# Kernel tuning notes

Measured on AMD Instinct MI355X. Metric: run time of the kernel, lower is better.

## Reference

```python
import jax, jax.numpy as jnp
import numpy as np

B, S, D = 4, 2048, 1024
H, E = 16, 64  # n_heads, head_size; H*E == D


def setup_inputs() -> dict:
    key = jax.random.key(0)
    ks = jax.random.split(key, 6)
    sd = 1.0 / np.sqrt(D)
    x = jax.random.normal(ks[0], (B, S, D), dtype=jnp.float32)
    # per-head Q/K/V projection weights, stacked: [H, D, E]
    Wq = jax.random.uniform(ks[1], (H, D, E), jnp.float32, -sd, sd)
    Wk = jax.random.uniform(ks[2], (H, D, E), jnp.float32, -sd, sd)
    Wv = jax.random.uniform(ks[3], (H, D, E), jnp.float32, -sd, sd)
    Wp = jax.random.uniform(ks[4], (D, D), jnp.float32, -sd, sd)
    bp = jax.random.uniform(ks[5], (D,), jnp.float32, -sd, sd)
    return {"x": x, "Wq": Wq, "Wk": Wk, "Wv": Wv, "Wp": Wp, "bp": bp}


def reference(x, Wq, Wk, Wv, Wp, bp):
    # Per-head projections (all heads batched): [B, H, S, E]
    q = jnp.einsum('bsd,hde->bhse', x, Wq)
    k = jnp.einsum('bsd,hde->bhse', x, Wk)
    v = jnp.einsum('bsd,hde->bhse', x, Wv)
    scale = E ** -0.5
    # Full causal score matrix [B, H, S, S]
    wei = jnp.einsum('bhse,bhte->bhst', q, k) * scale
    causal = jnp.tril(jnp.ones((S, S), dtype=bool))
    wei = jnp.where(causal, wei, -jnp.inf)
    wei = jax.nn.softmax(wei, axis=-1)
    out = jnp.einsum('bhst,bhte->bhse', wei, v)
    # concat heads along feature dim: [B, S, H*E]
    out = out.transpose(0, 2, 1, 3).reshape(B, S, H * E)
    # output projection (dropout is identity in eval)
    return out @ Wp.T + bp
```

## Files before the change

### kernel.cpp

```cpp
#include <hip/hip_runtime.h>

#define B_ 4
#define S_ 2048
#define D_ 1024
#define H_ 16
#define E_ 64
#define M_ (B_*S_)

typedef __attribute__((ext_vector_type(8))) short short8;
typedef __attribute__((ext_vector_type(4))) float floatx4;

#define GLD16(g, l) __builtin_amdgcn_global_load_lds( \
    (const __attribute__((address_space(1))) unsigned*)(g), \
    (__attribute__((address_space(3))) unsigned*)(l), 16, 0, 0)

__device__ __forceinline__ ushort f2b(float f) {
    union { float f; unsigned u; } v; v.f = f;
    unsigned r = v.u + 0x7fffu + ((v.u >> 16) & 1u);
    return (ushort)(r >> 16);
}
__device__ __forceinline__ unsigned cvt_pk_bf16(float lo, float hi) {
    unsigned r;
    asm("v_cvt_pk_bf16_f32 %0, %1, %2" : "=v"(r) : "v"(lo), "v"(hi));
    return r;
}
__device__ __forceinline__ float fast_exp2(float x) {
#if __has_builtin(__builtin_amdgcn_exp2f)
    return __builtin_amdgcn_exp2f(x);
#else
    float r; asm("v_exp_f32 %0, %1" : "=v"(r) : "v"(x)); return r;
#endif
}
__device__ __forceinline__ float lane_pull(float v, int srclane) {
    return __int_as_float(__builtin_amdgcn_ds_bpermute(srclane << 2, __float_as_int(v)));
}

__global__ __launch_bounds__(256) void prologue(const float* __restrict__ x,
                                                const float* __restrict__ Wq,
                                                const float* __restrict__ Wk,
                                                const float* __restrict__ Wv,
                                                const float* __restrict__ Wp,
                                                ushort* __restrict__ xb,
                                                ushort* __restrict__ wpb,
                                                ushort* __restrict__ wt) {
    __shared__ __align__(16) ushort T[64 * 80];
    const int bid = blockIdx.x;
    const int t = threadIdx.x;

    if (bid < 2048) {
        const int n8 = (int)((size_t)M_ * D_ / 8);
        int i = bid * 256 + t;
        const int stride = 2048 * 256;
        for (; i < n8; i += stride) {
            float4 a = ((const float4*)x)[2 * i];
            float4 b = ((const float4*)x)[2 * i + 1];
            short8 o;
            o[0] = (short)f2b(a.x); o[1] = (short)f2b(a.y);
            o[2] = (short)f2b(a.z); o[3] = (short)f2b(a.w);
            o[4] = (short)f2b(b.x); o[5] = (short)f2b(b.y);
            o[6] = (short)f2b(b.z); o[7] = (short)f2b(b.w);
            ((short8*)xb)[i] = o;
        }
    } else if (bid < 2560) {
        int i = (bid - 2048) * 256 + t;
        float4 a = ((const float4*)Wp)[2 * i];
        float4 b = ((const float4*)Wp)[2 * i + 1];
        short8 o;
        o[0] = (short)f2b(a.x); o[1] = (short)f2b(a.y);
        o[2] = (short)f2b(a.z); o[3] = (short)f2b(a.w);
        o[4] = (short)f2b(b.x); o[5] = (short)f2b(b.y);
        o[6] = (short)f2b(b.z); o[7] = (short)f2b(b.w);
        ((short8*)wpb)[i] = o;
    } else {
        const int q = bid - 2560;
        const int g = q >> 4;
        const int d0 = (q & 15) * 64;
        const float* W = (g < 16 ? Wq : (g < 32 ? Wk : Wv)) + (size_t)(g & 15) * (D_ * E_);
        #pragma unroll
        for (int it = 0; it < 4; ++it) {
            int i = it * 256 + t;
            int r = i >> 4, c = i & 15;
            float4 xx = *(const float4*)(W + (size_t)(d0 + r) * E_ + c * 4);
            T[(c * 4 + 0) * 80 + r] = f2b(xx.x);
            T[(c * 4 + 1) * 80 + r] = f2b(xx.y);
            T[(c * 4 + 2) * 80 + r] = f2b(xx.z);
            T[(c * 4 + 3) * 80 + r] = f2b(xx.w);
        }
        __syncthreads();
        #pragma unroll
        for (int it = 0; it < 2; ++it) {
            int i = it * 256 + t;
            int e = i >> 3, c = i & 7;
            short8 xx = *(const short8*)&T[e * 80 + c * 8];
            *(short8*)&wt[((size_t)g * E_ + e) * D_ + d0 + c * 8] = xx;
        }
    }
}

__global__ __launch_bounds__(512) void gemm_qkv(const ushort* __restrict__ xb,
                                                const ushort* __restrict__ wt,
                                                ushort* __restrict__ qk,
                                                ushort* __restrict__ vt) {
    const int m0 = blockIdx.x * 256;
    const int n0 = blockIdx.y * 128;
    const int w  = n0 >> 10;

    __shared__ __align__(16) ushort As[256 * 32];
    __shared__ __align__(16) ushort Bs[128 * 32];

    const int t = threadIdx.x, l = t & 63, wid = t >> 6;
    const int wm = (wid & 3) * 64, wn = (wid >> 2) * 64;
    floatx4 acc[4][4] = {};

    for (int k0 = 0; k0 < D_; k0 += 32) {
        __syncthreads();
        #pragma unroll
        for (int it = 0; it < 2; ++it) {
            int i = it * 512 + t;
            int r = i >> 2, cs = i & 3;
            int c = cs ^ ((r >> 1) & 3);
            GLD16(xb + (size_t)(m0 + r) * D_ + k0 + c * 8, &As[i * 8]);
        }
        {
            int r = t >> 2, cs = t & 3;
            int c = cs ^ ((r >> 1) & 3);
            GLD16(wt + (size_t)(n0 + r) * D_ + k0 + c * 8, &Bs[t * 8]);
        }
        __syncthreads();

        short8 af[4], bf[4];
        #pragma unroll
        for (int mf = 0; mf < 4; ++mf) {
            int row = wm + 16 * mf + (l & 15);
            int c = (l >> 4) ^ ((row >> 1) & 3);
            af[mf] = *(const short8*)&As[row * 32 + c * 8];
        }
        #pragma unroll
        for (int nf = 0; nf < 4; ++nf) {
            int row = wn + 16 * nf + (l & 15);
            int c = (l >> 4) ^ ((row >> 1) & 3);
            bf[nf] = *(const short8*)&Bs[row * 32 + c * 8];
        }
        #pragma unroll
        for (int mf = 0; mf < 4; ++mf)
            #pragma unroll
            for (int nf = 0; nf < 4; ++nf)
                acc[mf][nf] = __builtin_amdgcn_mfma_f32_16x16x32_bf16(af[mf], bf[nf], acc[mf][nf], 0, 0, 0);
    }

    if (w < 2) {
        ushort* outw = qk + (size_t)w * ((size_t)B_ * H_ * S_ * E_);
        #pragma unroll
        for (int mf = 0; mf < 4; ++mf)
            #pragma unroll
            for (int nf = 0; nf < 4; ++nf) {
                int n = n0 + wn + 16 * nf + (l & 15);
                int h = (n >> 6) & 15, e = n & 63;
                #pragma unroll
                for (int r = 0; r < 4; ++r) {
                    int m = m0 + wm + 16 * mf + (l >> 4) * 4 + r;
                    int b = m >> 11, s = m & (S_ - 1);
                    outw[((size_t)((b << 4) + h) * S_ + s) * E_ + e] = f2b(acc[mf][nf][r]);
                }
            }
    } else {
        #pragma unroll
        for (int mf = 0; mf < 4; ++mf) {
            int m = m0 + wm + 16 * mf + (l >> 4) * 4;
            int b = m >> 11, s = m & (S_ - 1);
            #pragma unroll
            for (int nf = 0; nf < 4; ++nf) {
                int n = n0 + wn + 16 * nf + (l & 15);
                int h = (n >> 6) & 15, e = n & 63;
                unsigned pk0 = cvt_pk_bf16(acc[mf][nf][0], acc[mf][nf][1]);
                unsigned pk1 = cvt_pk_bf16(acc[mf][nf][2], acc[mf][nf][3]);
                *(uint2*)&vt[((size_t)((b << 4) + h) * E_ + e) * S_ + s] = make_uint2(pk0, pk1);
            }
        }
    }
}

__global__ __launch_bounds__(256) void flash(const ushort* __restrict__ qg,
                                             const ushort* __restrict__ kg,
                                             const ushort* __restrict__ vtg,
                                             ushort* __restrict__ attn) {
    const int n = blockIdx.x;
    const int x = n >> 6;
    const int bh = n & 63;
    const int b = bh >> 4, h = bh & 15;
    const ushort* qb = qg + (size_t)bh * (S_ * E_);
    const ushort* kb = kg + (size_t)bh * (S_ * E_);
    const ushort* vb = vtg + (size_t)bh * (E_ * S_);

    __shared__ __align__(16) ushort QP[64 * 64];
    __shared__ __align__(16) ushort Ks[2][64 * 64];
    __shared__ __align__(16) ushort Vs[2][64 * 64];

    const int t = threadIdx.x, l = t & 63, wid = t >> 6;
    const float SC = 0.18033688f;
    const float NEG_INF = -__builtin_inff();
    const int g = l >> 4;
    const int qloc = l & 15;
    const int qts[2] = {x, 31 - x};
    ushort* Pw = &QP[wid * 1024];

    #pragma unroll 1
    for (int qi = 0; qi < 2; ++qi) {
        const int qt = qts[qi];

        #pragma unroll
        for (int it = 0; it < 2; ++it) {
            int i = it * 256 + t;
            int r = i >> 3, cs = i & 7, c = cs ^ (r & 7);
            GLD16(qb + (size_t)(qt * 64 + r) * E_ + c * 8, &QP[i * 8]);
            GLD16(kb + (size_t)r * E_ + c * 8, &Ks[0][i * 8]);
            GLD16(vb + (size_t)r * S_ + c * 8, &Vs[0][i * 8]);
        }
        __syncthreads();

        short8 qf[2];
        #pragma unroll
        for (int ks = 0; ks < 2; ++ks) {
            int row = wid * 16 + qloc;
            int c = (g + 4 * ks) ^ (row & 7);
            qf[ks] = *(const short8*)&QP[row * 64 + c * 8];
        }

        floatx4 o[4] = {};
        float mr = NEG_INF, lr = 0.f;

        int buf = 0;
        for (int jt = 0; jt <= qt; ++jt) {
            if (jt < qt) {
                #pragma unroll
                for (int it = 0; it < 2; ++it) {
                    int i = it * 256 + t;
                    int r = i >> 3, cs = i & 7, c = cs ^ (r & 7);
                    GLD16(kb + (size_t)((jt + 1) * 64 + r) * E_ + c * 8, &Ks[buf ^ 1][i * 8]);
                    GLD16(vb + (size_t)r * S_ + (jt + 1) * 64 + c * 8, &Vs[buf ^ 1][i * 8]);
                }
            }

            floatx4 s[4] = {};
            #pragma unroll
            for (int nf = 0; nf < 4; ++nf) {
                #pragma unroll
                for (int ks = 0; ks < 2; ++ks) {
                    int row = 16 * nf + qloc;
                    int c = (g + 4 * ks) ^ (row & 7);
                    short8 kf = *(const short8*)&Ks[buf][row * 64 + c * 8];
                    s[nf] = __builtin_amdgcn_mfma_f32_16x16x32_bf16(kf, qf[ks], s[nf], 0, 0, 0);
                }
            }

            if (jt == qt) {
                int qrow = wid * 16 + qloc;
                #pragma unroll
                for (int nf = 0; nf < 4; ++nf)
                    #pragma unroll
                    for (int r = 0; r < 4; ++r)
                        if (16 * nf + 4 * g + r > qrow) s[nf][r] = NEG_INF;
            }

            float mx = s[0][0];
            #pragma unroll
            for (int nf = 0; nf < 4; ++nf)
                #pragma unroll
                for (int r = 0; r < 4; ++r) mx = fmaxf(mx, s[nf][r]);
            mx = fmaxf(mx, __shfl_xor(mx, 16));
            mx = fmaxf(mx, __shfl_xor(mx, 32));
            bool ok = (mx - mr) * SC <= 8.0f;

            if (!__all(ok)) {
                float mn = fmaxf(mr, mx);
                float al = fast_exp2((mr - mn) * SC);
                mr = mn;
                lr *= al;
                #pragma unroll
                for (int r = 0; r < 4; ++r) {
                    float alq = lane_pull(al, 4 * g + r);
                    #pragma unroll
                    for (int nf = 0; nf < 4; ++nf) o[nf][r] *= alq;
                }
            }

            {
                float nm = -mr * SC;
                float rs = 0.f;
                #pragma unroll
                for (int nf = 0; nf < 4; ++nf)
                    #pragma unroll
                    for (int r = 0; r < 4; ++r) {
                        float p = fast_exp2(fmaf(s[nf][r], SC, nm));
                        s[nf][r] = p;
                        rs += p;
                    }
                lr += rs;
            }

            #pragma unroll
            for (int nf = 0; nf < 4; ++nf) {
                unsigned pk0 = cvt_pk_bf16(s[nf][0], s[nf][1]);
                unsigned pk1 = cvt_pk_bf16(s[nf][2], s[nf][3]);
                int chunk = 2 * nf + (g >> 1);
                int sw = chunk ^ (qloc & 7);
                int a = qloc * 64 + sw * 8 + 4 * (g & 1);
                *(uint2*)&Pw[a] = make_uint2(pk0, pk1);
            }

            short8 pf[2];
            #pragma unroll
            for (int ks = 0; ks < 2; ++ks) {
                int row = l & 15;
                int c = (g + 4 * ks) ^ (row & 7);
                pf[ks] = *(const short8*)&Pw[row * 64 + c * 8];
            }
            #pragma unroll
            for (int nf = 0; nf < 4; ++nf) {
                #pragma unroll
                for (int ks = 0; ks < 2; ++ks) {
                    int row = 16 * nf + (l & 15);
                    int c = (g + 4 * ks) ^ (row & 7);
                    short8 vf = *(const short8*)&Vs[buf][row * 64 + c * 8];
                    o[nf] = __builtin_amdgcn_mfma_f32_16x16x32_bf16(pf[ks], vf, o[nf], 0, 0, 0);
                }
            }

            __syncthreads();
            buf ^= 1;
        }

        lr += __shfl_xor(lr, 16);
        lr += __shfl_xor(lr, 32);
        float inv = 1.0f / lr;
        float il[4];
        #pragma unroll
        for (int r = 0; r < 4; ++r) il[r] = lane_pull(inv, 4 * g + r);

        #pragma unroll
        for (int nf = 0; nf < 4; ++nf) {
            int col = 16 * nf + qloc;
            #pragma unroll
            for (int rp = 0; rp < 2; ++rp) {
                unsigned pk = cvt_pk_bf16(o[nf][2 * rp] * il[2 * rp],
                                          o[nf][2 * rp + 1] * il[2 * rp + 1]);
                int row0 = g * 4 + 2 * rp;
                int a0 = row0 * 64 + (((col >> 3)) ^ (row0 & 7)) * 8 + (col & 7);
                int a1 = (row0 + 1) * 64 + (((col >> 3)) ^ ((row0 + 1) & 7)) * 8 + (col & 7);
                Pw[a0] = (ushort)pk;
                Pw[a1] = (ushort)(pk >> 16);
            }
        }
        #pragma unroll
        for (int it = 0; it < 2; ++it) {
            int i = it * 64 + l;
            int row = i >> 3, cc = i & 7;
            int c = cc ^ (row & 7);
            short8 vv = *(const short8*)&Pw[row * 64 + c * 8];
            int s_abs = qt * 64 + wid * 16 + row;
            *(short8*)&attn[((size_t)(b * S_ + s_abs)) * D_ + h * E_ + cc * 8] = vv;
        }
        __syncthreads();
    }
}

__global__ __launch_bounds__(256) void out_proj(const ushort* __restrict__ a,
                                                const ushort* __restrict__ wpb,
                                                const float* __restrict__ bp,
                                                float* __restrict__ out) {
    const int m0 = blockIdx.x * 128;
    const int n0 = blockIdx.y * 128;

    __shared__ __align__(16) ushort As[128 * 32];
    __shared__ __align__(16) ushort Bs[128 * 32];

    const int t = threadIdx.x, l = t & 63, wid = t >> 6;
    const int wm = (wid & 1) * 64, wn = (wid >> 1) * 64;
    floatx4 acc[4][4] = {};

    for (int k0 = 0; k0 < D_; k0 += 32) {
        __syncthreads();
        #pragma unroll
        for (int it = 0; it < 2; ++it) {
            int i = it * 256 + t;
            int r = i >> 2, cs = i & 3;
            int c = cs ^ ((r >> 1) & 3);
            GLD16(a + (size_t)(m0 + r) * D_ + k0 + c * 8, &As[i * 8]);
            GLD16(wpb + (size_t)(n0 + r) * D_ + k0 + c * 8, &Bs[i * 8]);
        }
        __syncthreads();

        short8 af[4], bf[4];
        #pragma unroll
        for (int mf = 0; mf < 4; ++mf) {
            int row = wm + 16 * mf + (l & 15);
            int c = (l >> 4) ^ ((row >> 1) & 3);
            af[mf] = *(const short8*)&As[row * 32 + c * 8];
        }
        #pragma unroll
        for (int nf = 0; nf < 4; ++nf) {
            int row = wn + 16 * nf + (l & 15);
            int c = (l >> 4) ^ ((row >> 1) & 3);
            bf[nf] = *(const short8*)&Bs[row * 32 + c * 8];
        }
        #pragma unroll
        for (int mf = 0; mf < 4; ++mf)
            #pragma unroll
            for (int nf = 0; nf < 4; ++nf)
                acc[mf][nf] = __builtin_amdgcn_mfma_f32_16x16x32_bf16(af[mf], bf[nf], acc[mf][nf], 0, 0, 0);
    }

    #pragma unroll
    for (int nf = 0; nf < 4; ++nf) {
        int col = n0 + wn + 16 * nf + (l & 15);
        float bias = bp[col];
        #pragma unroll
        for (int mf = 0; mf < 4; ++mf)
            #pragma unroll
            for (int r = 0; r < 4; ++r) {
                int m = m0 + wm + 16 * mf + (l >> 4) * 4 + r;
                out[(size_t)m * D_ + col] = acc[mf][nf][r] + bias;
            }
    }
}

extern "C" void kernel_launch(void* const* d_in, const int* in_sizes, int n_in,
                              void* d_out, int out_size, void* d_ws, size_t ws_size,
                              hipStream_t stream) {
    const float* x  = (const float*)d_in[0];
    const float* Wq = (const float*)d_in[1];
    const float* Wk = (const float*)d_in[2];
    const float* Wv = (const float*)d_in[3];
    const float* Wp = (const float*)d_in[4];
    const float* bp = (const float*)d_in[5];

    ushort* ws = (ushort*)d_ws;
    const size_t NX  = (size_t)M_ * D_;
    const size_t NW  = (size_t)48 * E_ * D_;
    const size_t NP  = (size_t)D_ * D_;
    const size_t QSZ = (size_t)B_ * H_ * S_ * E_;
    ushort* xb    = ws;
    ushort* wt    = xb + NX;
    ushort* wpb   = wt + NW;
    ushort* qk    = wpb + NP;
    ushort* vt    = qk + 2 * QSZ;
    ushort* attnb = vt + QSZ;

    prologue <<<3328, 256, 0, stream>>>(x, Wq, Wk, Wv, Wp, xb, wpb, wt);
    gemm_qkv <<<dim3(M_ / 256, 24), 512, 0, stream>>>(xb, wt, qk, vt);
    flash    <<<1024, 256, 0, stream>>>(qk, qk + QSZ, vt, attnb);
    out_proj <<<dim3(M_ / 128, D_ / 128), 256, 0, stream>>>(attnb, wpb, bp, (float*)d_out);
}
```

Baseline: 181.7 us.

## Double-buffer LDS tiles in QKV and output projection GEMMs

Converts the K-loop of the QKV projection GEMM and the output projection GEMM to double-buffered shared memory. The next K tile is prefetched with global_load_lds into the alternate buffer while MFMAs consume the current one, and the per-iteration syncs drop from two to one. This aims to hide global-load latency behind compute, at the cost of doubling LDS use per block, which may lower occupancy. The async LDS loads rely on the single barrier to drain them before the buffer swap.

After: 177.3 us (median of 2 runs). 2.4% less time.

```diff
diff --git a/kernel.cpp b/kernel.cpp
--- a/kernel.cpp
+++ b/kernel.cpp
@@ -105,47 +105,63 @@
     const int n0 = blockIdx.y * 128;
     const int w  = n0 >> 10;
 
-    __shared__ __align__(16) ushort As[256 * 32];
-    __shared__ __align__(16) ushort Bs[128 * 32];
+    __shared__ __align__(16) ushort As[2][256 * 32];
+    __shared__ __align__(16) ushort Bs[2][128 * 32];
 
     const int t = threadIdx.x, l = t & 63, wid = t >> 6;
     const int wm = (wid & 3) * 64, wn = (wid >> 2) * 64;
     floatx4 acc[4][4] = {};
 
-    for (int k0 = 0; k0 < D_; k0 += 32) {
-        __syncthreads();
+    {
         #pragma unroll
         for (int it = 0; it < 2; ++it) {
             int i = it * 512 + t;
             int r = i >> 2, cs = i & 3;
             int c = cs ^ ((r >> 1) & 3);
-            GLD16(xb + (size_t)(m0 + r) * D_ + k0 + c * 8, &As[i * 8]);
-        }
-        {
+            GLD16(xb + (size_t)(m0 + r) * D_ + c * 8, &As[0][i * 8]);
+        }
+        int r = t >> 2, cs = t & 3;
+        int c = cs ^ ((r >> 1) & 3);
+        GLD16(wt + (size_t)(n0 + r) * D_ + c * 8, &Bs[0][t * 8]);
+    }
+    __syncthreads();
+
+    int buf = 0;
+    for (int k0 = 0; k0 < D_; k0 += 32) {
+        if (k0 + 32 < D_) {
+            #pragma unroll
+            for (int it = 0; it < 2; ++it) {
+                int i = it * 512 + t;
+                int r = i >> 2, cs = i & 3;
+                int c = cs ^ ((r >> 1) & 3);
+                GLD16(xb + (size_t)(m0 + r) * D_ + k0 + 32 + c * 8, &As[buf ^ 1][i * 8]);
+            }
             int r = t >> 2, cs = t & 3;
             int c = cs ^ ((r >> 1) & 3);
-            GLD16(wt + (size_t)(n0 + r) * D_ + k0 + c * 8, &Bs[t * 8]);
-        }
-        __syncthreads();
+            GLD16(wt + (size_t)(n0 + r) * D_ + k0 + 32 + c * 8, &Bs[buf ^ 1][t * 8]);
+        }
 
         short8 af[4], bf[4];
         #pragma unroll
         for (int mf = 0; mf < 4; ++mf) {
             int row = wm + 16 * mf + (l & 15);
             int c = (l >> 4) ^ ((row >> 1) & 3);
-            af[mf] = *(const short8*)&As[row * 32 + c * 8];
+            af[mf] = *(const short8*)&As[buf][row * 32 + c * 8];
         }
         #pragma unroll
         for (int nf = 0; nf < 4; ++nf) {
             int row = wn + 16 * nf + (l & 15);
             int c = (l >> 4) ^ ((row >> 1) & 3);
-            bf[nf] = *(const short8*)&Bs[row * 32 + c * 8];
+            bf[nf] = *(const short8*)&Bs[buf][row * 32 + c * 8];
         }
         #pragma unroll
         for (int mf = 0; mf < 4; ++mf)
             #pragma unroll
             for (int nf = 0; nf < 4; ++nf)
                 acc[mf][nf] = __builtin_amdgcn_mfma_f32_16x16x32_bf16(af[mf], bf[nf], acc[mf][nf], 0, 0, 0);
+
+        __syncthreads();
+        buf ^= 1;
     }
 
     if (w < 2) {
@@ -371,43 +387,57 @@
     const int m0 = blockIdx.x * 128;
     const int n0 = blockIdx.y * 128;
 
-    __shared__ __align__(16) ushort As[128 * 32];
-    __shared__ __align__(16) ushort Bs[128 * 32];
+    __shared__ __align__(16) ushort As[2][128 * 32];
+    __shared__ __align__(16) ushort Bs[2][128 * 32];
 
     const int t = threadIdx.x, l = t & 63, wid = t >> 6;
     const int wm = (wid & 1) * 64, wn = (wid >> 1) * 64;
     floatx4 acc[4][4] = {};
 
+    #pragma unroll
+    for (int it = 0; it < 2; ++it) {
+        int i = it * 256 + t;
+        int r = i >> 2, cs = i & 3;
+        int c = cs ^ ((r >> 1) & 3);
+        GLD16(a + (size_t)(m0 + r) * D_ + c * 8, &As[0][i * 8]);
+        GLD16(wpb + (size_t)(n0 + r) * D_ + c * 8, &Bs[0][i * 8]);
+    }
+    __syncthreads();
+
+    int buf = 0;
     for (int k0 = 0; k0 < D_; k0 += 32) {
-        __syncthreads();
-        #pragma unroll
-        for (int it = 0; it < 2; ++it) {
-            int i = it * 256 + t;
-            int r = i >> 2, cs = i & 3;
-            int c = cs ^ ((r >> 1) & 3);
-            GLD16(a + (size_t)(m0 + r) * D_ + k0 + c * 8, &As[i * 8]);
-            GLD16(wpb + (size_t)(n0 + r) * D_ + k0 + c * 8, &Bs[i * 8]);
-        }
-        __syncthreads();
+        if (k0 + 32 < D_) {
+            #pragma unroll
+            for (int it = 0; it < 2; ++it) {
+                int i = it * 256 + t;
+                int r = i >> 2, cs = i & 3;
+                int c = cs ^ ((r >> 1) & 3);
+                GLD16(a + (size_t)(m0 + r) * D_ + k0 + 32 + c * 8, &As[buf ^ 1][i * 8]);
+                GLD16(wpb + (size_t)(n0 + r) * D_ + k0 + 32 + c * 8, &Bs[buf ^ 1][i * 8]);
+            }
+        }
 
         short8 af[4], bf[4];
         #pragma unroll
         for (int mf = 0; mf < 4; ++mf) {
             int row = wm + 16 * mf + (l & 15);
             int c = (l >> 4) ^ ((row >> 1) & 3);
-            af[mf] = *(const short8*)&As[row * 32 + c * 8];
+            af[mf] = *(const short8*)&As[buf][row * 32 + c * 8];
         }
         #pragma unroll
         for (int nf = 0; nf < 4; ++nf) {
             int row = wn + 16 * nf + (l & 15);
             int c = (l >> 4) ^ ((row >> 1) & 3);
-            bf[nf] = *(const short8*)&Bs[row * 32 + c * 8];
+            bf[nf] = *(const short8*)&Bs[buf][row * 32 + c * 8];
         }
         #pragma unroll
         for (int mf = 0; mf < 4; ++mf)
             #pragma unroll
             for (int nf = 0; nf < 4; ++nf)
                 acc[mf][nf] = __builtin_amdgcn_mfma_f32_16x16x32_bf16(af[mf], bf[nf], acc[mf][nf], 0, 0, 0);
+
+        __syncthreads();
+        buf ^= 1;
     }
 
     #pragma unroll
```
